# Kernel tuning notes

Measured on AMD Instinct MI355X. Metric: run time of the kernel, lower is better.

Reference implementation:

```python
import jax, jax.numpy as jnp
import numpy as np
import math

B, S, D, H = 4, 2048, 1024, 16
HD = D // H  # 64
FF = 4096
EPS = 1e-5


def layer_norm(x, g, b):
    mu = jnp.mean(x, axis=-1, keepdims=True)
    var = jnp.mean(jnp.square(x - mu), axis=-1, keepdims=True)
    return (x - mu) * jax.lax.rsqrt(var + EPS) * g + b


def setup_inputs() -> dict:
    key = jax.random.key(0)
    ks = jax.random.split(key, 16)
    sc = 0.02
    return {
        "x": jax.random.normal(ks[0], (B, S, D), dtype=jnp.float32),
        "Wq": jax.random.normal(ks[1], (H, D, HD), dtype=jnp.float32) * sc,
        "bq": jnp.zeros((H, HD), dtype=jnp.float32),
        "Wk": jax.random.normal(ks[2], (H, D, HD), dtype=jnp.float32) * sc,
        "bk": jnp.zeros((H, HD), dtype=jnp.float32),
        "Wv": jax.random.normal(ks[3], (H, D, HD), dtype=jnp.float32) * sc,
        "bv": jnp.zeros((H, HD), dtype=jnp.float32),
        "Wo": jax.random.normal(ks[4], (D, D), dtype=jnp.float32) * sc,
        "bo": jnp.zeros((D,), dtype=jnp.float32),
        "W1": jax.random.normal(ks[5], (D, FF), dtype=jnp.float32) * sc,
        "b1": jnp.zeros((FF,), dtype=jnp.float32),
        "W2": jax.random.normal(ks[6], (FF, D), dtype=jnp.float32) * sc,
        "b2": jnp.zeros((D,), dtype=jnp.float32),
        "ln1_g": jnp.ones((D,), dtype=jnp.float32),
        "ln1_b": jnp.zeros((D,), dtype=jnp.float32),
        "ln2_g": jnp.ones((D,), dtype=jnp.float32),
        "ln2_b": jnp.zeros((D,), dtype=jnp.float32),
    }


def reference(x, Wq, bq, Wk, bk, Wv, bv, Wo, bo, W1, b1, W2, b2, ln1_g, ln1_b, ln2_g, ln2_b):
    b, s, d = x.shape
    h1 = layer_norm(x, ln1_g, ln1_b)
    # per-head Q/K/V linears, vectorized over heads: [b,h,s,hd]
    q = jnp.einsum('bsd,hde->bhse', h1, Wq) + bq[None, :, None, :]
    k = jnp.einsum('bsd,hde->bhse', h1, Wk) + bk[None, :, None, :]
    v = jnp.einsum('bsd,hde->bhse', h1, Wv) + bv[None, :, None, :]
    scores = jnp.einsum('bhqe,bhke->bhqk', q, k) / math.sqrt(q.shape[-1])
    causal = jnp.tril(jnp.ones((s, s), dtype=bool))
    scores = jnp.where(causal[None, None], scores, -jnp.inf)
    weights = jax.nn.softmax(scores, axis=-1)
    attn = jnp.einsum('bhqk,bhke->bhqe', weights, v)
    # concat heads (head order = torch concat dim=-1)
    attn = attn.transpose(0, 2, 1, 3).reshape(b, s, d)
    x = x + attn @ Wo + bo
    h2 = layer_norm(x, ln2_g, ln2_b)
    y = jax.nn.gelu(h2 @ W1 + b1, approximate=False)
    y = jax.nn.gelu(y @ W2 + b2, approximate=False)
    return x + y
```

## Files before the change

kernel.cpp:

```cpp
#include <hip/hip_runtime.h>
#include <cstdint>
#include <cstddef>


#define DI __device__ __forceinline__

typedef __attribute__((ext_vector_type(8))) __bf16 bf16x8;
typedef __attribute__((ext_vector_type(4))) float floatx4;

static constexpr int Bn = 4, Sn = 2048, Dn = 1024, Hn = 16, HDn = 64, FFn = 4096;
static constexpr int NTOK = Bn * Sn;
static constexpr int D3 = 3 * Dn;

DI float bf2f(unsigned short u) { return __uint_as_float(((unsigned int)u) << 16); }
DI unsigned short f2bf(float f) {
  unsigned int u = __float_as_uint(f);
  u += 0x7FFFu + ((u >> 16) & 1u);
  return (unsigned short)(u >> 16);
}
DI float gelu_f(float v) { return 0.5f * v * (1.0f + erff(v * 0.70710678118654752f)); }
DI bf16x8 ld8(const unsigned short* p) { return *(const bf16x8*)p; }
DI floatx4 mfma16(bf16x8 a, bf16x8 b, floatx4 c) {
  return __builtin_amdgcn_mfma_f32_16x16x32_bf16(a, b, c, 0, 0, 0);
}
DI void g2l16(const unsigned short* g, unsigned short* l) {
  __builtin_amdgcn_global_load_lds((__attribute__((address_space(1))) void*)g,
                                   (__attribute__((address_space(3))) void*)l,
                                   16, 0, 0);
}
DI float ldin(const void* p, size_t idx, bool f32) {
  return f32 ? ((const float*)p)[idx] : bf2f(((const unsigned short*)p)[idx]);
}
DI int swz16(int row, int col) {
  return (row << 6) + ((((col >> 3) ^ row ^ (row >> 3)) & 7) << 3) + (col & 7);
}

__global__ void detect_kernel(const unsigned short* __restrict__ x,
                              int* __restrict__ flag) {
  int t = threadIdx.x;
  int cnt = 0;
  for (int i = t; i < 1024; i += 64) {
    unsigned short u = x[2 * i];
    int e = (u >> 7) & 0xFF;
    cnt += (e >= 96 && e <= 142) ? 1 : 0;
  }
  #pragma unroll
  for (int off = 32; off >= 1; off >>= 1) cnt += __shfl_xor(cnt, off);
  if (t == 0) *flag = (cnt < 820) ? 1 : 0;
}

__global__ void vec_prep(const void* bq, const void* bk, const void* bv,
                         const void* bo, const void* b1, const void* b2,
                         const void* g1, const void* be1, const void* g2,
                         const void* be2, unsigned short* __restrict__ dst,
                         const int* __restrict__ flag) {
  int i = blockIdx.x * 256 + threadIdx.x;
  if (i >= 13312) return;
  const bool f32 = *flag != 0;
  const void* src; int off;
  if      (i < 1024)  { src = bq;  off = i; }
  else if (i < 2048)  { src = bk;  off = i - 1024; }
  else if (i < 3072)  { src = bv;  off = i - 2048; }
  else if (i < 4096)  { src = bo;  off = i - 3072; }
  else if (i < 8192)  { src = b1;  off = i - 4096; }
  else if (i < 9216)  { src = b2;  off = i - 8192; }
  else if (i < 10240) { src = g1;  off = i - 9216; }
  else if (i < 11264) { src = be1; off = i - 10240; }
  else if (i < 12288) { src = g2;  off = i - 11264; }
  else                { src = be2; off = i - 12288; }
  dst[i] = f2bf(ldin(src, off, f32));
}

__global__ void transpose_kernel(const void* __restrict__ src,
                                 unsigned short* __restrict__ dst, int K, int N,
                                 const int* __restrict__ flag) {
  __shared__ unsigned short tile[64][65];
  const bool f32 = *flag != 0;
  int kb = blockIdx.y * 64, nb = blockIdx.x * 64;
  for (int i = threadIdx.x; i < 4096; i += 256) {
    int r = i >> 6, c = i & 63;
    tile[r][c] = f2bf(ldin(src, (size_t)(kb + r) * N + nb + c, f32));
  }
  __syncthreads();
  for (int i = threadIdx.x; i < 4096; i += 256) {
    int r = i >> 6, c = i & 63;
    dst[(size_t)(nb + r) * K + kb + c] = tile[c][r];
  }
}

__global__ void qkvT_kernel(const void* __restrict__ Wq,
                            const void* __restrict__ Wk,
                            const void* __restrict__ Wv,
                            unsigned short* __restrict__ WT,
                            const int* __restrict__ flag) {
  __shared__ unsigned short tile[64][65];
  const bool f32 = *flag != 0;
  const void* src = blockIdx.z == 0 ? Wq : (blockIdx.z == 1 ? Wk : Wv);
  int h = blockIdx.y, d0 = blockIdx.x * 64;
  size_t base = (size_t)h * (Dn * HDn);
  for (int i = threadIdx.x; i < 4096; i += 256) {
    int r = i >> 6, c = i & 63;
    tile[r][c] = f2bf(ldin(src, base + (size_t)(d0 + r) * 64 + c, f32));
  }
  __syncthreads();
  for (int i = threadIdx.x; i < 4096; i += 256) {
    int r = i >> 6, c = i & 63;
    WT[(size_t)(blockIdx.z * 1024 + h * 64 + r) * 1024 + d0 + c] = tile[c][r];
  }
}

__global__ __launch_bounds__(256) void ln_kernel(const void* __restrict__ x,
                                                 const unsigned short* __restrict__ g,
                                                 const unsigned short* __restrict__ b,
                                                 unsigned short* __restrict__ out,
                                                 const int* __restrict__ flag) {
  const bool f32 = flag ? (*flag != 0) : true;
  int row = blockIdx.x, t = threadIdx.x;
  float v[4];
  if (f32) {
    float4 f = *(const float4*)((const float*)x + (size_t)row * Dn + t * 4);
    v[0] = f.x; v[1] = f.y; v[2] = f.z; v[3] = f.w;
  } else {
    ushort4 u = *(const ushort4*)((const unsigned short*)x + (size_t)row * Dn + t * 4);
    v[0] = bf2f(u.x); v[1] = bf2f(u.y); v[2] = bf2f(u.z); v[3] = bf2f(u.w);
  }
  float s = v[0] + v[1] + v[2] + v[3];
  float s2 = v[0] * v[0] + v[1] * v[1] + v[2] * v[2] + v[3] * v[3];
  #pragma unroll
  for (int off = 32; off >= 1; off >>= 1) {
    s += __shfl_xor(s, off);
    s2 += __shfl_xor(s2, off);
  }
  __shared__ float red[8];
  int wv = t >> 6, ln = t & 63;
  if (ln == 0) { red[wv] = s; red[4 + wv] = s2; }
  __syncthreads();
  s = red[0] + red[1] + red[2] + red[3];
  s2 = red[4] + red[5] + red[6] + red[7];
  float mu = s * (1.0f / 1024.0f);
  float var = s2 * (1.0f / 1024.0f) - mu * mu;
  float rs = rsqrtf(fmaxf(var, 0.0f) + 1e-5f);
  ushort4 gg = *(const ushort4*)(g + t * 4);
  ushort4 bb = *(const ushort4*)(b + t * 4);
  ushort4 o;
  o.x = f2bf((v[0] - mu) * rs * bf2f(gg.x) + bf2f(bb.x));
  o.y = f2bf((v[1] - mu) * rs * bf2f(gg.y) + bf2f(bb.y));
  o.z = f2bf((v[2] - mu) * rs * bf2f(gg.z) + bf2f(bb.z));
  o.w = f2bf((v[3] - mu) * rs * bf2f(gg.w) + bf2f(bb.w));
  *(ushort4*)(out + (size_t)row * Dn + t * 4) = o;
}

enum { EPI_BIAS_BF16 = 0, EPI_WO = 1, EPI_GELU = 2, EPI_FF2 = 3 };

template <int EPI>
__global__ __launch_bounds__(256, 2) void gemm_kernel(
    const unsigned short* __restrict__ A, const unsigned short* __restrict__ BT,
    const unsigned short* __restrict__ bias, const void* __restrict__ residv,
    const float* __restrict__ resid_f, unsigned short* __restrict__ Cb,
    float* __restrict__ Cf, const int* __restrict__ flag, int M, int N, int K) {
  __shared__ unsigned short As[128 * 32];
  __shared__ unsigned short Bs[128 * 32];
  const int m0 = blockIdx.y * 128, n0 = blockIdx.x * 128;
  const int w = threadIdx.x >> 6, lane = threadIdx.x & 63;
  const int waveM = (w >> 1) * 64, waveN = (w & 1) * 64;
  const int m16 = lane & 15, quad = lane >> 4;
  const bool rf32 = flag && (*flag != 0);

  const int srow = w * 32 + (lane >> 2);
  const int scol = (lane & 3) * 8;
  const unsigned short* Ag = A + (size_t)(m0 + srow) * K + scol;
  const unsigned short* Bg = BT + (size_t)(n0 + srow) * K + scol;
  unsigned short* Al = As + srow * 32 + scol;
  unsigned short* Bl = Bs + srow * 32 + scol;
  const size_t rowstep = (size_t)16 * K;

  floatx4 acc[4][4];
  #pragma unroll
  for (int i = 0; i < 4; i++)
    #pragma unroll
    for (int j = 0; j < 4; j++) acc[i][j] = floatx4{0.f, 0.f, 0.f, 0.f};

  for (int k0 = 0; k0 < K; k0 += 32) {
    g2l16(Ag, Al);
    g2l16(Ag + rowstep, Al + 16 * 32);
    g2l16(Bg, Bl);
    g2l16(Bg + rowstep, Bl + 16 * 32);
    Ag += 32; Bg += 32;
    __syncthreads();
    bf16x8 af[4], bfv[4];
    #pragma unroll
    for (int mt = 0; mt < 4; mt++)
      af[mt] = ld8(As + (waveM + mt * 16 + m16) * 32 + quad * 8);
    #pragma unroll
    for (int nt = 0; nt < 4; nt++)
      bfv[nt] = ld8(Bs + (waveN + nt * 16 + m16) * 32 + quad * 8);
    #pragma unroll
    for (int mt = 0; mt < 4; mt++)
      #pragma unroll
      for (int nt = 0; nt < 4; nt++)
        acc[mt][nt] = mfma16(af[mt], bfv[nt], acc[mt][nt]);
    __syncthreads();
  }

  #pragma unroll
  for (int mt = 0; mt < 4; mt++) {
    #pragma unroll
    for (int nt = 0; nt < 4; nt++) {
      const int col = n0 + waveN + nt * 16 + m16;
      const float bcol = bf2f(bias[col]);
      #pragma unroll
      for (int r = 0; r < 4; r++) {
        const int row = m0 + waveM + mt * 16 + quad * 4 + r;
        const size_t idx = (size_t)row * N + col;
        float v = acc[mt][nt][r] + bcol;
        if constexpr (EPI == EPI_BIAS_BF16) {
          Cb[idx] = f2bf(v);
        } else if constexpr (EPI == EPI_WO) {
          float rv = rf32 ? ((const float*)residv)[idx]
                          : bf2f(((const unsigned short*)residv)[idx]);
          Cf[idx] = v + rv;
        } else if constexpr (EPI == EPI_GELU) {
          Cb[idx] = f2bf(gelu_f(v));
        } else {
          float ov = gelu_f(v) + resid_f[idx];
          if (rf32) Cf[idx] = ov;
          else      Cb[idx] = f2bf(ov);
        }
      }
    }
  }
}

__global__ __launch_bounds__(256, 4) void attn_kernel(
    const unsigned short* __restrict__ qkv, unsigned short* __restrict__ attn) {
  const int qt = (int)gridDim.x - 1 - (int)blockIdx.x;
  const int bh = blockIdx.y;
  const int b = bh >> 4, h = bh & 15;
  const int w = threadIdx.x >> 6, lane = threadIdx.x & 63;
  const int m16 = lane & 15, quad = lane >> 4;

  __shared__ unsigned short Ks[64 * 64];
  __shared__ unsigned short Vt[64 * 64];
  __shared__ unsigned short Ps[4 * 16 * 64];
  unsigned short* PsW = Ps + w * 16 * 64;

  const int qrow = qt * 64 + w * 16 + m16;
  const unsigned short* qp = qkv + (size_t)(b * Sn + qrow) * D3 + h * 64 + quad * 8;
  const bf16x8 qf0 = ld8(qp), qf1 = ld8(qp + 32);

  floatx4 acc_o[4];
  #pragma unroll
  for (int nt = 0; nt < 4; nt++) acc_o[nt] = floatx4{0.f, 0.f, 0.f, 0.f};
  float lsum[4] = {0.f, 0.f, 0.f, 0.f};

  for (int kt = 0; kt <= qt; ++kt) {
    __syncthreads();
    {
      const size_t kvbase = (size_t)(b * Sn + kt * 64) * D3 + h * 64;
      #pragma unroll
      for (int i = 0; i < 2; i++) {
        int j = threadIdx.x + i * 256;
        int krow = j >> 3, c = j & 7;
        const unsigned short* kp = qkv + kvbase + (size_t)krow * D3 + 1024 + c * 8;
        *(uint4*)(Ks + swz16(krow, c * 8)) = *(const uint4*)kp;
        const unsigned short* vp = qkv + kvbase + (size_t)krow * D3 + 2048 + c * 8;
        uint4 vv = *(const uint4*)vp;
        unsigned short tmp[8];
        *(uint4*)tmp = vv;
        #pragma unroll
        for (int e = 0; e < 8; e++) Vt[swz16(c * 8 + e, krow)] = tmp[e];
      }
    }
    __syncthreads();

    floatx4 sa[4];
    #pragma unroll
    for (int nt = 0; nt < 4; nt++) {
      sa[nt] = floatx4{0.f, 0.f, 0.f, 0.f};
      bf16x8 k0 = ld8(Ks + swz16(nt * 16 + m16, quad * 8));
      bf16x8 k1 = ld8(Ks + swz16(nt * 16 + m16, 32 + quad * 8));
      sa[nt] = mfma16(qf0, k0, sa[nt]);
      sa[nt] = mfma16(qf1, k1, sa[nt]);
    }

    #pragma unroll
    for (int r = 0; r < 4; r++) {
      const int qg = qt * 64 + w * 16 + quad * 4 + r;
      #pragma unroll
      for (int nt = 0; nt < 4; nt++) {
        const int kg = kt * 64 + nt * 16 + m16;
        float p = (kg <= qg) ? __expf(sa[nt][r] * 0.125f) : 0.0f;
        lsum[r] += p;
        PsW[swz16(quad * 4 + r, nt * 16 + m16)] = f2bf(p);
      }
    }
    const bf16x8 p0 = ld8(PsW + swz16(m16, quad * 8));
    const bf16x8 p1 = ld8(PsW + swz16(m16, 32 + quad * 8));
    #pragma unroll
    for (int nt = 0; nt < 4; nt++) {
      bf16x8 v0 = ld8(Vt + swz16(nt * 16 + m16, quad * 8));
      bf16x8 v1 = ld8(Vt + swz16(nt * 16 + m16, 32 + quad * 8));
      acc_o[nt] = mfma16(p0, v0, acc_o[nt]);
      acc_o[nt] = mfma16(p1, v1, acc_o[nt]);
    }
  }

  #pragma unroll
  for (int r = 0; r < 4; r++) {
    #pragma unroll
    for (int off = 1; off < 16; off <<= 1) lsum[r] += __shfl_xor(lsum[r], off);
  }

  #pragma unroll
  for (int r = 0; r < 4; r++) {
    const float inv = 1.0f / fmaxf(lsum[r], 1e-20f);
    const size_t orow = (size_t)(b * Sn + qt * 64 + w * 16 + quad * 4 + r) * Dn + h * 64;
    #pragma unroll
    for (int nt = 0; nt < 4; nt++)
      attn[orow + nt * 16 + m16] = f2bf(acc_o[nt][r] * inv);
  }
}

extern "C" void kernel_launch(void* const* d_in, const int* in_sizes, int n_in,
                              void* d_out, int out_size, void* d_ws, size_t ws_size,
                              hipStream_t stream) {
  (void)in_sizes; (void)n_in; (void)out_size; (void)ws_size;
  const void* x    = d_in[0];
  const void* Wq   = d_in[1];
  const void* bq   = d_in[2];
  const void* Wk   = d_in[3];
  const void* bk   = d_in[4];
  const void* Wv   = d_in[5];
  const void* bv   = d_in[6];
  const void* Wo   = d_in[7];
  const void* bo   = d_in[8];
  const void* W1   = d_in[9];
  const void* b1   = d_in[10];
  const void* W2   = d_in[11];
  const void* b2   = d_in[12];
  const void* ln1g = d_in[13];
  const void* ln1b = d_in[14];
  const void* ln2g = d_in[15];
  const void* ln2b = d_in[16];
  char* ws = (char*)d_ws;

  constexpr size_t OFF_WTQKV = 0;
  constexpr size_t OFF_WOT   = OFF_WTQKV + (size_t)D3 * Dn * 2;
  constexpr size_t OFF_W1T   = OFF_WOT + (size_t)Dn * Dn * 2;
  constexpr size_t OFF_W2T   = OFF_W1T + (size_t)FFn * Dn * 2;
  constexpr size_t OFF_VEC   = OFF_W2T + (size_t)Dn * FFn * 2;
  constexpr size_t OFF_FLAG  = OFF_VEC + 32768;
  constexpr size_t OFF_H     = OFF_FLAG + 256;
  constexpr size_t OFF_QKV   = OFF_H + (size_t)NTOK * Dn * 2;
  constexpr size_t OFF_ATTN  = OFF_QKV + (size_t)NTOK * D3 * 2;
  constexpr size_t OFF_X2    = OFF_ATTN + (size_t)NTOK * Dn * 2;
  constexpr size_t OFF_Y1    = OFF_QKV;

  unsigned short* WTqkv = (unsigned short*)(ws + OFF_WTQKV);
  unsigned short* WoT   = (unsigned short*)(ws + OFF_WOT);
  unsigned short* W1T   = (unsigned short*)(ws + OFF_W1T);
  unsigned short* W2T   = (unsigned short*)(ws + OFF_W2T);
  unsigned short* vec   = (unsigned short*)(ws + OFF_VEC);
  int*            flag  = (int*)(ws + OFF_FLAG);
  unsigned short* hbuf  = (unsigned short*)(ws + OFF_H);
  unsigned short* qkvb  = (unsigned short*)(ws + OFF_QKV);
  unsigned short* attnb = (unsigned short*)(ws + OFF_ATTN);
  float*          x2    = (float*)(ws + OFF_X2);
  unsigned short* y1    = (unsigned short*)(ws + OFF_Y1);

  detect_kernel<<<1, 64, 0, stream>>>((const unsigned short*)x, flag);

  vec_prep<<<52, 256, 0, stream>>>(bq, bk, bv, bo, b1, b2, ln1g, ln1b, ln2g,
                                   ln2b, vec, flag);
  qkvT_kernel<<<dim3(16, 16, 3), 256, 0, stream>>>(Wq, Wk, Wv, WTqkv, flag);
  transpose_kernel<<<dim3(16, 16), 256, 0, stream>>>(Wo, WoT, 1024, 1024, flag);
  transpose_kernel<<<dim3(64, 16), 256, 0, stream>>>(W1, W1T, 1024, 4096, flag);
  transpose_kernel<<<dim3(16, 64), 256, 0, stream>>>(W2, W2T, 4096, 1024, flag);

  ln_kernel<<<NTOK, 256, 0, stream>>>(x, vec + 9216, vec + 10240, hbuf, flag);
  gemm_kernel<EPI_BIAS_BF16><<<dim3(D3 / 128, NTOK / 128), 256, 0, stream>>>(
      hbuf, WTqkv, vec + 0, nullptr, nullptr, qkvb, nullptr, nullptr,
      NTOK, D3, Dn);
  attn_kernel<<<dim3(Sn / 64, Bn * Hn), 256, 0, stream>>>(qkvb, attnb);
  gemm_kernel<EPI_WO><<<dim3(Dn / 128, NTOK / 128), 256, 0, stream>>>(
      attnb, WoT, vec + 3072, x, nullptr, nullptr, x2, flag, NTOK, Dn, Dn);
  ln_kernel<<<NTOK, 256, 0, stream>>>(x2, vec + 11264, vec + 12288, hbuf, nullptr);
  gemm_kernel<EPI_GELU><<<dim3(FFn / 128, NTOK / 128), 256, 0, stream>>>(
      hbuf, W1T, vec + 4096, nullptr, nullptr, y1, nullptr, nullptr,
      NTOK, FFn, Dn);
  gemm_kernel<EPI_FF2><<<dim3(Dn / 128, NTOK / 128), 256, 0, stream>>>(
      y1, W2T, vec + 8192, nullptr, x2, (unsigned short*)d_out, (float*)d_out,
      flag, NTOK, Dn, FFn);
}
```

Baseline: 671.4 us.

## Write K/V pre-tiled and swizzled from QKV GEMM; widen attention query tile

The QKV GEMM epilogue now writes Q row-major, and writes K and V straight into per-(batch, head, key-tile) 64x64 blocks that are already swizzled, with V stored transposed. The attention kernel can then copy whole K/V tiles into LDS with contiguous 16-byte copies instead of strided loads plus a scalar transpose scatter. Each attention block now handles 128 queries (two 16-row MFMA tiles per wave), so every loaded K/V tile is reused twice as much. The GEMM launch bound also rises to 3 waves-per-EU occupancy, which may increase register pressure, and the strided scattered stores in the QKV epilogue may cost some write efficiency.

```diff
diff --git a/kernel.cpp b/kernel.cpp
--- a/kernel.cpp
+++ b/kernel.cpp
@@ -150,14 +150,16 @@
   *(ushort4*)(out + (size_t)row * Dn + t * 4) = o;
 }
 
-enum { EPI_BIAS_BF16 = 0, EPI_WO = 1, EPI_GELU = 2, EPI_FF2 = 3 };
+enum { EPI_QKV = 0, EPI_WO = 1, EPI_GELU = 2, EPI_FF2 = 3 };
 
 template <int EPI>
-__global__ __launch_bounds__(256, 2) void gemm_kernel(
+__global__ __launch_bounds__(256, 3) void gemm_kernel(
     const unsigned short* __restrict__ A, const unsigned short* __restrict__ BT,
     const unsigned short* __restrict__ bias, const void* __restrict__ residv,
     const float* __restrict__ resid_f, unsigned short* __restrict__ Cb,
-    float* __restrict__ Cf, const int* __restrict__ flag, int M, int N, int K) {
+    float* __restrict__ Cf, unsigned short* __restrict__ Ck,
+    unsigned short* __restrict__ Cv, const int* __restrict__ flag,
+    int M, int N, int K) {
   __shared__ unsigned short As[128 * 32];
   __shared__ unsigned short Bs[128 * 32];
   const int m0 = blockIdx.y * 128, n0 = blockIdx.x * 128;
@@ -208,23 +210,51 @@
     for (int nt = 0; nt < 4; nt++) {
       const int col = n0 + waveN + nt * 16 + m16;
       const float bcol = bf2f(bias[col]);
-      #pragma unroll
-      for (int r = 0; r < 4; r++) {
-        const int row = m0 + waveM + mt * 16 + quad * 4 + r;
-        const size_t idx = (size_t)row * N + col;
-        float v = acc[mt][nt][r] + bcol;
-        if constexpr (EPI == EPI_BIAS_BF16) {
-          Cb[idx] = f2bf(v);
-        } else if constexpr (EPI == EPI_WO) {
-          float rv = rf32 ? ((const float*)residv)[idx]
-                          : bf2f(((const unsigned short*)residv)[idx]);
-          Cf[idx] = v + rv;
-        } else if constexpr (EPI == EPI_GELU) {
-          Cb[idx] = f2bf(gelu_f(v));
+      const int row0 = m0 + waveM + mt * 16 + quad * 4;
+      if constexpr (EPI == EPI_QKV) {
+        const int region = n0 >> 10;
+        if (region == 0) {
+          #pragma unroll
+          for (int r = 0; r < 4; r++)
+            Cb[(size_t)(row0 + r) * 1024 + col] = f2bf(acc[mt][nt][r] + bcol);
+        } else if (region == 1) {
+          const int co = col - 1024, h = co >> 6, e = co & 63;
+          const int b = row0 >> 11;
+          #pragma unroll
+          for (int r = 0; r < 4; r++) {
+            const int s = (row0 + r) & 2047, kt = s >> 6, kr = s & 63;
+            const size_t tb = (size_t)((b * 16 + h) * 32 + kt) * 4096;
+            Ck[tb + swz16(kr, e)] = f2bf(acc[mt][nt][r] + bcol);
+          }
         } else {
-          float ov = gelu_f(v) + resid_f[idx];
-          if (rf32) Cf[idx] = ov;
-          else      Cb[idx] = f2bf(ov);
+          const int co = col - 2048, h = co >> 6, e = co & 63;
+          const int b = row0 >> 11;
+          const int s0 = row0 & 2047, kt = s0 >> 6, kr0 = s0 & 63;
+          const size_t tb = (size_t)((b * 16 + h) * 32 + kt) * 4096;
+          ushort4 o;
+          o.x = f2bf(acc[mt][nt][0] + bcol);
+          o.y = f2bf(acc[mt][nt][1] + bcol);
+          o.z = f2bf(acc[mt][nt][2] + bcol);
+          o.w = f2bf(acc[mt][nt][3] + bcol);
+          *(ushort4*)(Cv + tb + (e << 6) +
+                      ((((kr0 >> 3) ^ e ^ (e >> 3)) & 7) << 3) + (kr0 & 7)) = o;
+        }
+      } else {
+        #pragma unroll
+        for (int r = 0; r < 4; r++) {
+          const size_t idx = (size_t)(row0 + r) * N + col;
+          float v = acc[mt][nt][r] + bcol;
+          if constexpr (EPI == EPI_WO) {
+            float rv = rf32 ? ((const float*)residv)[idx]
+                            : bf2f(((const unsigned short*)residv)[idx]);
+            Cf[idx] = v + rv;
+          } else if constexpr (EPI == EPI_GELU) {
+            Cb[idx] = f2bf(gelu_f(v));
+          } else {
+            float ov = gelu_f(v) + resid_f[idx];
+            if (rf32) Cf[idx] = ov;
+            else      Cb[idx] = f2bf(ov);
+          }
         }
       }
     }
@@ -232,7 +262,8 @@
 }
 
 __global__ __launch_bounds__(256, 4) void attn_kernel(
-    const unsigned short* __restrict__ qkv, unsigned short* __restrict__ attn) {
+    const unsigned short* __restrict__ qg, const unsigned short* __restrict__ kg,
+    const unsigned short* __restrict__ vg, unsigned short* __restrict__ attn) {
   const int qt = (int)gridDim.x - 1 - (int)blockIdx.x;
   const int bh = blockIdx.y;
   const int b = bh >> 4, h = bh & 15;
@@ -241,84 +272,105 @@
 
   __shared__ unsigned short Ks[64 * 64];
   __shared__ unsigned short Vt[64 * 64];
-  __shared__ unsigned short Ps[4 * 16 * 64];
-  unsigned short* PsW = Ps + w * 16 * 64;
-
-  const int qrow = qt * 64 + w * 16 + m16;
-  const unsigned short* qp = qkv + (size_t)(b * Sn + qrow) * D3 + h * 64 + quad * 8;
-  const bf16x8 qf0 = ld8(qp), qf1 = ld8(qp + 32);
-
-  floatx4 acc_o[4];
-  #pragma unroll
-  for (int nt = 0; nt < 4; nt++) acc_o[nt] = floatx4{0.f, 0.f, 0.f, 0.f};
-  float lsum[4] = {0.f, 0.f, 0.f, 0.f};
-
-  for (int kt = 0; kt <= qt; ++kt) {
+  __shared__ unsigned short Ps[4 * 32 * 64];
+  unsigned short* PsW = Ps + w * 32 * 64;
+
+  bf16x8 qf[2][2];
+  #pragma unroll
+  for (int mt = 0; mt < 2; mt++) {
+    const int qrow = qt * 128 + w * 32 + mt * 16 + m16;
+    const unsigned short* qp = qg + (size_t)(b * Sn + qrow) * Dn + h * 64 + quad * 8;
+    qf[mt][0] = ld8(qp);
+    qf[mt][1] = ld8(qp + 32);
+  }
+
+  floatx4 acc_o[2][4];
+  float lsum[2][4];
+  #pragma unroll
+  for (int mt = 0; mt < 2; mt++)
+    #pragma unroll
+    for (int nt = 0; nt < 4; nt++) {
+      acc_o[mt][nt] = floatx4{0.f, 0.f, 0.f, 0.f};
+      lsum[mt][nt & 3] = 0.f;
+    }
+
+  const int c0 = threadIdx.x * 8;
+  const int c1 = c0 + 256 * 8;
+  const int ktmax = 2 * qt + 1;
+  for (int kt = 0; kt <= ktmax; ++kt) {
     __syncthreads();
-    {
-      const size_t kvbase = (size_t)(b * Sn + kt * 64) * D3 + h * 64;
-      #pragma unroll
-      for (int i = 0; i < 2; i++) {
-        int j = threadIdx.x + i * 256;
-        int krow = j >> 3, c = j & 7;
-        const unsigned short* kp = qkv + kvbase + (size_t)krow * D3 + 1024 + c * 8;
-        *(uint4*)(Ks + swz16(krow, c * 8)) = *(const uint4*)kp;
-        const unsigned short* vp = qkv + kvbase + (size_t)krow * D3 + 2048 + c * 8;
-        uint4 vv = *(const uint4*)vp;
-        unsigned short tmp[8];
-        *(uint4*)tmp = vv;
-        #pragma unroll
-        for (int e = 0; e < 8; e++) Vt[swz16(c * 8 + e, krow)] = tmp[e];
-      }
-    }
+    const unsigned short* kb = kg + (size_t)(bh * 32 + kt) * 4096;
+    const unsigned short* vb = vg + (size_t)(bh * 32 + kt) * 4096;
+    g2l16(kb + c0, Ks + c0);
+    g2l16(kb + c1, Ks + c1);
+    g2l16(vb + c0, Vt + c0);
+    g2l16(vb + c1, Vt + c1);
     __syncthreads();
 
-    floatx4 sa[4];
+    floatx4 sa[2][4];
     #pragma unroll
     for (int nt = 0; nt < 4; nt++) {
-      sa[nt] = floatx4{0.f, 0.f, 0.f, 0.f};
       bf16x8 k0 = ld8(Ks + swz16(nt * 16 + m16, quad * 8));
       bf16x8 k1 = ld8(Ks + swz16(nt * 16 + m16, 32 + quad * 8));
-      sa[nt] = mfma16(qf0, k0, sa[nt]);
-      sa[nt] = mfma16(qf1, k1, sa[nt]);
-    }
-
-    #pragma unroll
-    for (int r = 0; r < 4; r++) {
-      const int qg = qt * 64 + w * 16 + quad * 4 + r;
-      #pragma unroll
-      for (int nt = 0; nt < 4; nt++) {
-        const int kg = kt * 64 + nt * 16 + m16;
-        float p = (kg <= qg) ? __expf(sa[nt][r] * 0.125f) : 0.0f;
-        lsum[r] += p;
-        PsW[swz16(quad * 4 + r, nt * 16 + m16)] = f2bf(p);
+      #pragma unroll
+      for (int mt = 0; mt < 2; mt++) {
+        floatx4 t = mfma16(qf[mt][0], k0, floatx4{0.f, 0.f, 0.f, 0.f});
+        sa[mt][nt] = mfma16(qf[mt][1], k1, t);
       }
     }
-    const bf16x8 p0 = ld8(PsW + swz16(m16, quad * 8));
-    const bf16x8 p1 = ld8(PsW + swz16(m16, 32 + quad * 8));
+
+    #pragma unroll
+    for (int mt = 0; mt < 2; mt++)
+      #pragma unroll
+      for (int r = 0; r < 4; r++) {
+        const int qgr = qt * 128 + w * 32 + mt * 16 + quad * 4 + r;
+        #pragma unroll
+        for (int nt = 0; nt < 4; nt++) {
+          const int kgc = kt * 64 + nt * 16 + m16;
+          float p = (kgc <= qgr) ? __expf(sa[mt][nt][r] * 0.125f) : 0.0f;
+          lsum[mt][r] += p;
+          PsW[swz16(mt * 16 + quad * 4 + r, nt * 16 + m16)] = f2bf(p);
+        }
+      }
+
+    bf16x8 pf[2][2];
+    #pragma unroll
+    for (int mt = 0; mt < 2; mt++) {
+      pf[mt][0] = ld8(PsW + swz16(mt * 16 + m16, quad * 8));
+      pf[mt][1] = ld8(PsW + swz16(mt * 16 + m16, 32 + quad * 8));
+    }
     #pragma unroll
     for (int nt = 0; nt < 4; nt++) {
       bf16x8 v0 = ld8(Vt + swz16(nt * 16 + m16, quad * 8));
       bf16x8 v1 = ld8(Vt + swz16(nt * 16 + m16, 32 + quad * 8));
-      acc_o[nt] = mfma16(p0, v0, acc_o[nt]);
-      acc_o[nt] = mfma16(p1, v1, acc_o[nt]);
-    }
-  }
-
-  #pragma unroll
-  for (int r = 0; r < 4; r++) {
-    #pragma unroll
-    for (int off = 1; off < 16; off <<= 1) lsum[r] += __shfl_xor(lsum[r], off);
-  }
-
-  #pragma unroll
-  for (int r = 0; r < 4; r++) {
-    const float inv = 1.0f / fmaxf(lsum[r], 1e-20f);
-    const size_t orow = (size_t)(b * Sn + qt * 64 + w * 16 + quad * 4 + r) * Dn + h * 64;
-    #pragma unroll
-    for (int nt = 0; nt < 4; nt++)
-      attn[orow + nt * 16 + m16] = f2bf(acc_o[nt][r] * inv);
-  }
+      #pragma unroll
+      for (int mt = 0; mt < 2; mt++) {
+        acc_o[mt][nt] = mfma16(pf[mt][0], v0, acc_o[mt][nt]);
+        acc_o[mt][nt] = mfma16(pf[mt][1], v1, acc_o[mt][nt]);
+      }
+    }
+  }
+
+  #pragma unroll
+  for (int mt = 0; mt < 2; mt++)
+    #pragma unroll
+    for (int r = 0; r < 4; r++) {
+      #pragma unroll
+      for (int off = 1; off < 16; off <<= 1)
+        lsum[mt][r] += __shfl_xor(lsum[mt][r], off);
+    }
+
+  #pragma unroll
+  for (int mt = 0; mt < 2; mt++)
+    #pragma unroll
+    for (int r = 0; r < 4; r++) {
+      const float inv = 1.0f / fmaxf(lsum[mt][r], 1e-20f);
+      const size_t orow =
+          (size_t)(b * Sn + qt * 128 + w * 32 + mt * 16 + quad * 4 + r) * Dn + h * 64;
+      #pragma unroll
+      for (int nt = 0; nt < 4; nt++)
+        attn[orow + nt * 16 + m16] = f2bf(acc_o[mt][nt][r] * inv);
+    }
 }
 
 extern "C" void kernel_launch(void* const* d_in, const int* in_sizes, int n_in,
@@ -363,7 +415,9 @@
   unsigned short* vec   = (unsigned short*)(ws + OFF_VEC);
   int*            flag  = (int*)(ws + OFF_FLAG);
   unsigned short* hbuf  = (unsigned short*)(ws + OFF_H);
-  unsigned short* qkvb  = (unsigned short*)(ws + OFF_QKV);
+  unsigned short* qg    = (unsigned short*)(ws + OFF_QKV);
+  unsigned short* kg    = qg + (size_t)NTOK * Dn;
+  unsigned short* vg    = kg + (size_t)NTOK * Dn;
   unsigned short* attnb = (unsigned short*)(ws + OFF_ATTN);
   float*          x2    = (float*)(ws + OFF_X2);
   unsigned short* y1    = (unsigned short*)(ws + OFF_Y1);
@@ -378,17 +432,18 @@
   transpose_kernel<<<dim3(16, 64), 256, 0, stream>>>(W2, W2T, 4096, 1024, flag);
 
   ln_kernel<<<NTOK, 256, 0, stream>>>(x, vec + 9216, vec + 10240, hbuf, flag);
-  gemm_kernel<EPI_BIAS_BF16><<<dim3(D3 / 128, NTOK / 128), 256, 0, stream>>>(
-      hbuf, WTqkv, vec + 0, nullptr, nullptr, qkvb, nullptr, nullptr,
+  gemm_kernel<EPI_QKV><<<dim3(D3 / 128, NTOK / 128), 256, 0, stream>>>(
+      hbuf, WTqkv, vec + 0, nullptr, nullptr, qg, nullptr, kg, vg, nullptr,
       NTOK, D3, Dn);
-  attn_kernel<<<dim3(Sn / 64, Bn * Hn), 256, 0, stream>>>(qkvb, attnb);
+  attn_kernel<<<dim3(Sn / 128, Bn * Hn), 256, 0, stream>>>(qg, kg, vg, attnb);
   gemm_kernel<EPI_WO><<<dim3(Dn / 128, NTOK / 128), 256, 0, stream>>>(
-      attnb, WoT, vec + 3072, x, nullptr, nullptr, x2, flag, NTOK, Dn, Dn);
+      attnb, WoT, vec + 3072, x, nullptr, nullptr, x2, nullptr, nullptr, flag,
+      NTOK, Dn, Dn);
   ln_kernel<<<NTOK, 256, 0, stream>>>(x2, vec + 11264, vec + 12288, hbuf, nullptr);
   gemm_kernel<EPI_GELU><<<dim3(FFn / 128, NTOK / 128), 256, 0, stream>>>(
-      hbuf, W1T, vec + 4096, nullptr, nullptr, y1, nullptr, nullptr,
-      NTOK, FFn, Dn);
+      hbuf, W1T, vec + 4096, nullptr, nullptr, y1, nullptr, nullptr, nullptr,
+      nullptr, NTOK, FFn, Dn);
   gemm_kernel<EPI_FF2><<<dim3(Dn / 128, NTOK / 128), 256, 0, stream>>>(
       y1, W2T, vec + 8192, nullptr, x2, (unsigned short*)d_out, (float*)d_out,
-      flag, NTOK, Dn, FFn);
-}
+      nullptr, nullptr, flag, NTOK, Dn, FFn);
+}
```

After: 800.1 us. 19.2% more time.

## Double-buffer attention K/V tiles with register prefetch and packed V transpose

Applied to the files above, without the earlier changes.

The attention kernel now prefetches the next K/V tile into registers while computing on the current one, and stores tiles into double-buffered shared memory, which drops one __syncthreads per iteration. The V transpose now writes packed 32-bit pairs instead of scalar 16-bit stores. The GEMM launch bounds also change from 2 to 3 blocks per SM. These changes aim to hide global load latency and cut LDS store count, at the cost of more registers and shared memory per block in attention and possible register pressure or spills in the GEMM.

```diff
diff --git a/kernel.cpp b/kernel.cpp
--- a/kernel.cpp
+++ b/kernel.cpp
@@ -153,7 +153,7 @@
 enum { EPI_BIAS_BF16 = 0, EPI_WO = 1, EPI_GELU = 2, EPI_FF2 = 3 };
 
 template <int EPI>
-__global__ __launch_bounds__(256, 2) void gemm_kernel(
+__global__ __launch_bounds__(256, 3) void gemm_kernel(
     const unsigned short* __restrict__ A, const unsigned short* __restrict__ BT,
     const unsigned short* __restrict__ bias, const void* __restrict__ residv,
     const float* __restrict__ resid_f, unsigned short* __restrict__ Cb,
@@ -236,13 +236,14 @@
   const int qt = (int)gridDim.x - 1 - (int)blockIdx.x;
   const int bh = blockIdx.y;
   const int b = bh >> 4, h = bh & 15;
-  const int w = threadIdx.x >> 6, lane = threadIdx.x & 63;
+  const int tid = threadIdx.x;
+  const int w = tid >> 6, lane = tid & 63;
   const int m16 = lane & 15, quad = lane >> 4;
 
-  __shared__ unsigned short Ks[64 * 64];
-  __shared__ unsigned short Vt[64 * 64];
-  __shared__ unsigned short Ps[4 * 16 * 64];
-  unsigned short* PsW = Ps + w * 16 * 64;
+  __shared__ unsigned short Ks[2][4096];
+  __shared__ unsigned short Vt[2][4096];
+  __shared__ unsigned short Ps[4][1024];
+  unsigned short* PsW = Ps[w];
 
   const int qrow = qt * 64 + w * 16 + m16;
   const unsigned short* qp = qkv + (size_t)(b * Sn + qrow) * D3 + h * 64 + quad * 8;
@@ -253,53 +254,68 @@
   for (int nt = 0; nt < 4; nt++) acc_o[nt] = floatx4{0.f, 0.f, 0.f, 0.f};
   float lsum[4] = {0.f, 0.f, 0.f, 0.f};
 
+  const int kr = tid >> 3, kc = (tid & 7) * 8;
+  const int vk = (tid >> 3) * 2, ve = (tid & 7) * 8;
+
+  uint4 kreg0, kreg1, vreg0, vreg1;
+  const unsigned short* const kvroot = qkv + (size_t)(b * Sn) * D3 + h * 64;
+
+  {
+    const unsigned short* base = kvroot;
+    kreg0 = *(const uint4*)(base + (size_t)kr * D3 + 1024 + kc);
+    kreg1 = *(const uint4*)(base + (size_t)(kr + 32) * D3 + 1024 + kc);
+    vreg0 = *(const uint4*)(base + (size_t)vk * D3 + 2048 + ve);
+    vreg1 = *(const uint4*)(base + (size_t)(vk + 1) * D3 + 2048 + ve);
+  }
+
   for (int kt = 0; kt <= qt; ++kt) {
+    const int pb = kt & 1;
+    *(uint4*)(Ks[pb] + swz16(kr, kc)) = kreg0;
+    *(uint4*)(Ks[pb] + swz16(kr + 32, kc)) = kreg1;
+    {
+      const unsigned short* a0 = (const unsigned short*)&vreg0;
+      const unsigned short* a1 = (const unsigned short*)&vreg1;
+      #pragma unroll
+      for (int i = 0; i < 8; i++) {
+        unsigned int word = (unsigned int)a0[i] | ((unsigned int)a1[i] << 16);
+        *(unsigned int*)(Vt[pb] + swz16(ve + i, vk)) = word;
+      }
+    }
     __syncthreads();
-    {
-      const size_t kvbase = (size_t)(b * Sn + kt * 64) * D3 + h * 64;
-      #pragma unroll
-      for (int i = 0; i < 2; i++) {
-        int j = threadIdx.x + i * 256;
-        int krow = j >> 3, c = j & 7;
-        const unsigned short* kp = qkv + kvbase + (size_t)krow * D3 + 1024 + c * 8;
-        *(uint4*)(Ks + swz16(krow, c * 8)) = *(const uint4*)kp;
-        const unsigned short* vp = qkv + kvbase + (size_t)krow * D3 + 2048 + c * 8;
-        uint4 vv = *(const uint4*)vp;
-        unsigned short tmp[8];
-        *(uint4*)tmp = vv;
-        #pragma unroll
-        for (int e = 0; e < 8; e++) Vt[swz16(c * 8 + e, krow)] = tmp[e];
-      }
-    }
-    __syncthreads();
+    if (kt < qt) {
+      const unsigned short* base = kvroot + (size_t)(kt + 1) * 64 * D3;
+      kreg0 = *(const uint4*)(base + (size_t)kr * D3 + 1024 + kc);
+      kreg1 = *(const uint4*)(base + (size_t)(kr + 32) * D3 + 1024 + kc);
+      vreg0 = *(const uint4*)(base + (size_t)vk * D3 + 2048 + ve);
+      vreg1 = *(const uint4*)(base + (size_t)(vk + 1) * D3 + 2048 + ve);
+    }
 
     floatx4 sa[4];
     #pragma unroll
     for (int nt = 0; nt < 4; nt++) {
-      sa[nt] = floatx4{0.f, 0.f, 0.f, 0.f};
-      bf16x8 k0 = ld8(Ks + swz16(nt * 16 + m16, quad * 8));
-      bf16x8 k1 = ld8(Ks + swz16(nt * 16 + m16, 32 + quad * 8));
-      sa[nt] = mfma16(qf0, k0, sa[nt]);
-      sa[nt] = mfma16(qf1, k1, sa[nt]);
+      bf16x8 k0 = ld8(Ks[pb] + swz16(nt * 16 + m16, quad * 8));
+      bf16x8 k1 = ld8(Ks[pb] + swz16(nt * 16 + m16, 32 + quad * 8));
+      floatx4 t = mfma16(qf0, k0, floatx4{0.f, 0.f, 0.f, 0.f});
+      sa[nt] = mfma16(qf1, k1, t);
     }
 
     #pragma unroll
     for (int r = 0; r < 4; r++) {
-      const int qg = qt * 64 + w * 16 + quad * 4 + r;
+      const int qgr = qt * 64 + w * 16 + quad * 4 + r;
       #pragma unroll
       for (int nt = 0; nt < 4; nt++) {
-        const int kg = kt * 64 + nt * 16 + m16;
-        float p = (kg <= qg) ? __expf(sa[nt][r] * 0.125f) : 0.0f;
-        lsum[r] += p;
-        PsW[swz16(quad * 4 + r, nt * 16 + m16)] = f2bf(p);
+        const int kgc = kt * 64 + nt * 16 + m16;
+        float pv = (kgc <= qgr) ? __expf(sa[nt][r] * 0.125f) : 0.0f;
+        lsum[r] += pv;
+        PsW[swz16(quad * 4 + r, nt * 16 + m16)] = f2bf(pv);
       }
     }
     const bf16x8 p0 = ld8(PsW + swz16(m16, quad * 8));
     const bf16x8 p1 = ld8(PsW + swz16(m16, 32 + quad * 8));
     #pragma unroll
     for (int nt = 0; nt < 4; nt++) {
-      bf16x8 v0 = ld8(Vt + swz16(nt * 16 + m16, quad * 8));
-      bf16x8 v1 = ld8(Vt + swz16(nt * 16 + m16, 32 + quad * 8));
+      bf16x8 v0 = ld8(Vt[pb] + swz16(nt * 16 + m16, quad * 8));
+      bf16x8 v1 = ld8(Vt[pb] + swz16(nt * 16 + m16, 32 + quad * 8));
       acc_o[nt] = mfma16(p0, v0, acc_o[nt]);
       acc_o[nt] = mfma16(p1, v1, acc_o[nt]);
     }
```

New measurement: 667.8 us. No clear change (-0.5%).
